# Kernel optimization log

Measured on AMD Instinct MI355X. Metric: run time of the kernel, lower is better.

The kernel has to match this reference:

```python
import jax, jax.numpy as jnp
import numpy as np

AVG_FRAMES_PER_PHONE = 8.0


def setup_inputs() -> dict:
    key = jax.random.key(0)
    k1, k2, k3 = jax.random.split(key, 3)
    B, K, D, T = 16, 512, 256, 4096
    # positive durations averaging ~8 frames per phoneme
    durations = jax.random.uniform(k1, (B, K), dtype=jnp.float32) * (2.0 * AVG_FRAMES_PER_PHONE)
    phoneme = jax.random.normal(k2, (B, D, K), dtype=jnp.float32)
    frame = jax.random.normal(k3, (B, D, T), dtype=jnp.float32)
    return {"durations": durations, "phoneme": phoneme, "frame": frame}


def reference(durations, phoneme, frame):
    """Learnable duration upsampler (NaturalSpeech-style soft alignment).

    durations: (B, K) float frames per phoneme
    phoneme:   (B, D, K)
    frame:     (B, D, T)
    """
    T = frame.shape[-1]
    acc = jnp.cumsum(durations, axis=-1)                 # (B, K) end boundaries
    centers = acc - 0.5 * durations                      # (B, K) phoneme centers
    t = jnp.arange(T, dtype=durations.dtype) + 0.5       # (T,) frame centers
    # energy: negative squared distance frame-center -> phoneme-center
    energy = -((t[None, :, None] - centers[:, None, :]) ** 2)   # (B, T, K)
    w = jax.nn.softmax(energy, axis=-1)                  # soft alignment (B, T, K)
    upsampled = jnp.einsum("btk,bdk->bdt", w, phoneme)   # (B, D, T)
    return upsampled + frame
```

## Files before the change

kernel.cpp:

```cpp
#include <hip/hip_runtime.h>
#include <hip/hip_bf16.h>

#define BK 512
#define BD 256
#define BT 4096
#define W  16
#define DSPLIT 16
#define ROWS (BD / DSPLIT)
#define SROWS 8
#define NSTAGE (ROWS / SROWS)
#define TSPAN 1024

typedef __attribute__((address_space(1))) const float gfloat;
typedef __attribute__((address_space(3))) float lfloat;
typedef float v2f __attribute__((ext_vector_type(2)));

__global__ __launch_bounds__(256, 4)
void upsampler_kernel(const float* __restrict__ durations,
                      const float* __restrict__ phoneme,
                      const float* __restrict__ frame,
                      float* __restrict__ out)
{
    const int b   = blockIdx.x;
    const int tt  = blockIdx.y;
    const int ds  = blockIdx.z;
    const int tid = threadIdx.x;

    __shared__ float s_c[BK];
    __shared__ float s_ph[2][SROWS * BK];
    __shared__ float s_wsum[4];

    const float d0v = durations[b * BK + 2 * tid];
    const float d1v = durations[b * BK + 2 * tid + 1];
    float scan = d0v + d1v;
    #pragma unroll
    for (int off = 1; off < 64; off <<= 1) {
        float other = __shfl_up(scan, off, 64);
        if ((tid & 63) >= off) scan += other;
    }
    if ((tid & 63) == 63) s_wsum[tid >> 6] = scan;
    __syncthreads();
    float woff = 0.f;
    const int wv = tid >> 6;
    for (int i = 0; i < wv; ++i) woff += s_wsum[i];
    const float acc1 = woff + scan;
    s_c[2 * tid]     = (acc1 - d1v) - 0.5f * d0v;
    s_c[2 * tid + 1] = acc1 - 0.5f * d1v;
    __syncthreads();

    const int   t0  = tt * TSPAN + 4 * tid;
    const float tcm = (float)t0 + 2.0f;

    int pos = 0;
    #pragma unroll
    for (int st = 256; st > 0; st >>= 1) {
        int np = pos + st;
        if (np <= BK && s_c[np - 1] < tcm) pos = np;
    }
    int wstart = (pos - 8) & ~3;
    wstart = max(0, min(BK - W, wstart));

    float e[4][W];
    float m[4] = {-1e30f, -1e30f, -1e30f, -1e30f};
    #pragma unroll
    for (int j = 0; j < W; ++j) {
        const float c = s_c[wstart + j];
        #pragma unroll
        for (int o = 0; o < 4; ++o) {
            float dd = ((float)t0 + 0.5f + (float)o) - c;
            e[o][j] = -dd * dd;
            m[o] = fmaxf(m[o], e[o][j]);
        }
    }
    float sum[4] = {0.f, 0.f, 0.f, 0.f};
    #pragma unroll
    for (int j = 0; j < W; ++j) {
        #pragma unroll
        for (int o = 0; o < 4; ++o) { e[o][j] = __expf(e[o][j] - m[o]); sum[o] += e[o][j]; }
    }
    v2f E[4][W / 2];
    #pragma unroll
    for (int o = 0; o < 4; ++o) {
        const float inv = 1.0f / sum[o];
        #pragma unroll
        for (int j = 0; j < W / 2; ++j)
            E[o][j] = (v2f){e[o][2 * j] * inv, e[o][2 * j + 1] * inv};
    }

    const int dlo = ds * ROWS;
    const float* phb  = phoneme + ((size_t)b * BD + dlo) * BK;
    const float* frb  = frame   + ((size_t)b * BD + dlo) * BT + (size_t)tt * TSPAN + 4 * tid;
    float*       outb = out     + ((size_t)b * BD + dlo) * BT + (size_t)tt * TSPAN + 4 * tid;

    {
        const float* gsrc = phb;
        #pragma unroll
        for (int c = 0; c < 4; ++c) {
            const int off = (c * 256 + tid) * 4;
            __builtin_amdgcn_global_load_lds((gfloat*)(gsrc + off),
                                             (lfloat*)(&s_ph[0][0] + off), 16, 0, 0);
        }
    }

    #pragma unroll
    for (int sg = 0; sg < NSTAGE; ++sg) {
        asm volatile("s_waitcnt vmcnt(0)" ::: "memory");
        __syncthreads();

        if (sg + 1 < NSTAGE) {
            const float* gsrc = phb + (size_t)(sg + 1) * SROWS * BK;
            #pragma unroll
            for (int c = 0; c < 4; ++c) {
                const int off = (c * 256 + tid) * 4;
                __builtin_amdgcn_global_load_lds((gfloat*)(gsrc + off),
                                                 (lfloat*)(&s_ph[(sg + 1) & 1][0] + off), 16, 0, 0);
            }
        }

        const float* bufp = &s_ph[sg & 1][0];
        #pragma unroll
        for (int r = 0; r < SROWS; ++r) {
            const int d = sg * SROWS + r;
            const float4 frv = *(const float4*)(frb + (size_t)d * BT);
            const float4* sp4 = (const float4*)(bufp + r * BK + wstart);
            v2f a0 = (v2f){0.f, 0.f}, a1 = a0, a2 = a0, a3 = a0;
            #pragma unroll
            for (int q = 0; q < W / 4; ++q) {
                float4 p = sp4[q];
                v2f lo = (v2f){p.x, p.y};
                v2f hi = (v2f){p.z, p.w};
                a0 = __builtin_elementwise_fma(E[0][2 * q], lo, a0);
                a0 = __builtin_elementwise_fma(E[0][2 * q + 1], hi, a0);
                a1 = __builtin_elementwise_fma(E[1][2 * q], lo, a1);
                a1 = __builtin_elementwise_fma(E[1][2 * q + 1], hi, a1);
                a2 = __builtin_elementwise_fma(E[2][2 * q], lo, a2);
                a2 = __builtin_elementwise_fma(E[2][2 * q + 1], hi, a2);
                a3 = __builtin_elementwise_fma(E[3][2 * q], lo, a3);
                a3 = __builtin_elementwise_fma(E[3][2 * q + 1], hi, a3);
            }
            float4 ov;
            ov.x = (a0.x + a0.y) + frv.x;
            ov.y = (a1.x + a1.y) + frv.y;
            ov.z = (a2.x + a2.y) + frv.z;
            ov.w = (a3.x + a3.y) + frv.w;
            *(float4*)(outb + (size_t)d * BT) = ov;
        }
    }
}

extern "C" void kernel_launch(void* const* d_in, const int* in_sizes, int n_in,
                              void* d_out, int out_size, void* d_ws, size_t ws_size,
                              hipStream_t stream) {
    const float* durations = (const float*)d_in[0];
    const float* phoneme   = (const float*)d_in[1];
    const float* frame     = (const float*)d_in[2];
    float* out = (float*)d_out;

    dim3 grid(16, BT / TSPAN, DSPLIT);
    upsampler_kernel<<<grid, 256, 0, stream>>>(durations, phoneme, frame, out);
}
```

Measured before the change: 127.1 us.

## Use 512-thread blocks with 2 frames per thread and single-stage phoneme load

Blocks grow to 512 threads, each handling 2 frame positions instead of 4, and the D dimension is split 32 ways so each block owns 8 rows. The phoneme slice is loaded into LDS in one shot, issued before the duration scan so it overlaps that work, replacing the double-buffered staged pipeline. Frame and output traffic moves from float4 to float2 accesses. The aim is more parallelism, fewer registers per thread and less synchronisation. The softmax weights are now computed by twice as many threads, and the narrower memory accesses may lower bandwidth efficiency.

```diff
diff --git a/kernel.cpp b/kernel.cpp
--- a/kernel.cpp
+++ b/kernel.cpp
@@ -1,21 +1,19 @@
 #include <hip/hip_runtime.h>
-#include <hip/hip_bf16.h>
 
 #define BK 512
 #define BD 256
 #define BT 4096
 #define W  16
-#define DSPLIT 16
+#define DSPLIT 32
 #define ROWS (BD / DSPLIT)
-#define SROWS 8
-#define NSTAGE (ROWS / SROWS)
-#define TSPAN 1024
+#define NTHR 512
+#define TSPAN (NTHR * 2)
 
 typedef __attribute__((address_space(1))) const float gfloat;
 typedef __attribute__((address_space(3))) float lfloat;
 typedef float v2f __attribute__((ext_vector_type(2)));
 
-__global__ __launch_bounds__(256, 4)
+__global__ __launch_bounds__(NTHR, 8)
 void upsampler_kernel(const float* __restrict__ durations,
                       const float* __restrict__ phoneme,
                       const float* __restrict__ frame,
@@ -27,12 +25,21 @@
     const int tid = threadIdx.x;
 
     __shared__ float s_c[BK];
-    __shared__ float s_ph[2][SROWS * BK];
-    __shared__ float s_wsum[4];
+    __shared__ float s_ph[ROWS * BK];
+    __shared__ float s_wsum[8];
 
-    const float d0v = durations[b * BK + 2 * tid];
-    const float d1v = durations[b * BK + 2 * tid + 1];
-    float scan = d0v + d1v;
+    const float d0v = durations[b * BK + tid];
+
+    const int dlo = ds * ROWS;
+    const float* phb = phoneme + ((size_t)b * BD + dlo) * BK;
+    #pragma unroll
+    for (int c = 0; c < 2; ++c) {
+        const int off = (c * NTHR + tid) * 4;
+        __builtin_amdgcn_global_load_lds((gfloat*)(phb + off),
+                                         (lfloat*)(&s_ph[0] + off), 16, 0, 0);
+    }
+
+    float scan = d0v;
     #pragma unroll
     for (int off = 1; off < 64; off <<= 1) {
         float other = __shfl_up(scan, off, 64);
@@ -43,13 +50,12 @@
     float woff = 0.f;
     const int wv = tid >> 6;
     for (int i = 0; i < wv; ++i) woff += s_wsum[i];
-    const float acc1 = woff + scan;
-    s_c[2 * tid]     = (acc1 - d1v) - 0.5f * d0v;
-    s_c[2 * tid + 1] = acc1 - 0.5f * d1v;
+    const float acc = woff + scan;
+    s_c[tid] = acc - 0.5f * d0v;
     __syncthreads();
 
-    const int   t0  = tt * TSPAN + 4 * tid;
-    const float tcm = (float)t0 + 2.0f;
+    const int   t0  = tt * TSPAN + 2 * tid;
+    const float tcm = (float)t0 + 1.0f;
 
     int pos = 0;
     #pragma unroll
@@ -60,91 +66,57 @@
     int wstart = (pos - 8) & ~3;
     wstart = max(0, min(BK - W, wstart));
 
-    float e[4][W];
-    float m[4] = {-1e30f, -1e30f, -1e30f, -1e30f};
+    float e0[W], e1[W];
+    float m0 = -1e30f, m1 = -1e30f;
     #pragma unroll
     for (int j = 0; j < W; ++j) {
         const float c = s_c[wstart + j];
-        #pragma unroll
-        for (int o = 0; o < 4; ++o) {
-            float dd = ((float)t0 + 0.5f + (float)o) - c;
-            e[o][j] = -dd * dd;
-            m[o] = fmaxf(m[o], e[o][j]);
-        }
+        const float da = ((float)t0 + 0.5f) - c;
+        const float db = da + 1.0f;
+        e0[j] = -da * da; m0 = fmaxf(m0, e0[j]);
+        e1[j] = -db * db; m1 = fmaxf(m1, e1[j]);
     }
-    float sum[4] = {0.f, 0.f, 0.f, 0.f};
+    float s0 = 0.f, s1 = 0.f;
     #pragma unroll
     for (int j = 0; j < W; ++j) {
+        e0[j] = __expf(e0[j] - m0); s0 += e0[j];
+        e1[j] = __expf(e1[j] - m1); s1 += e1[j];
+    }
+    v2f E0[W / 2], E1[W / 2];
+    {
+        const float i0 = 1.0f / s0, i1 = 1.0f / s1;
         #pragma unroll
-        for (int o = 0; o < 4; ++o) { e[o][j] = __expf(e[o][j] - m[o]); sum[o] += e[o][j]; }
-    }
-    v2f E[4][W / 2];
-    #pragma unroll
-    for (int o = 0; o < 4; ++o) {
-        const float inv = 1.0f / sum[o];
-        #pragma unroll
-        for (int j = 0; j < W / 2; ++j)
-            E[o][j] = (v2f){e[o][2 * j] * inv, e[o][2 * j + 1] * inv};
-    }
-
-    const int dlo = ds * ROWS;
-    const float* phb  = phoneme + ((size_t)b * BD + dlo) * BK;
-    const float* frb  = frame   + ((size_t)b * BD + dlo) * BT + (size_t)tt * TSPAN + 4 * tid;
-    float*       outb = out     + ((size_t)b * BD + dlo) * BT + (size_t)tt * TSPAN + 4 * tid;
-
-    {
-        const float* gsrc = phb;
-        #pragma unroll
-        for (int c = 0; c < 4; ++c) {
-            const int off = (c * 256 + tid) * 4;
-            __builtin_amdgcn_global_load_lds((gfloat*)(gsrc + off),
-                                             (lfloat*)(&s_ph[0][0] + off), 16, 0, 0);
+        for (int j = 0; j < W / 2; ++j) {
+            E0[j] = (v2f){e0[2 * j] * i0, e0[2 * j + 1] * i0};
+            E1[j] = (v2f){e1[2 * j] * i1, e1[2 * j + 1] * i1};
         }
     }
 
+    const float* frb  = frame + ((size_t)b * BD + dlo) * BT + (size_t)tt * TSPAN + 2 * tid;
+    float*       outb = out   + ((size_t)b * BD + dlo) * BT + (size_t)tt * TSPAN + 2 * tid;
+
+    asm volatile("s_waitcnt vmcnt(0)" ::: "memory");
+    __syncthreads();
+
     #pragma unroll
-    for (int sg = 0; sg < NSTAGE; ++sg) {
-        asm volatile("s_waitcnt vmcnt(0)" ::: "memory");
-        __syncthreads();
-
-        if (sg + 1 < NSTAGE) {
-            const float* gsrc = phb + (size_t)(sg + 1) * SROWS * BK;
-            #pragma unroll
-            for (int c = 0; c < 4; ++c) {
-                const int off = (c * 256 + tid) * 4;
-                __builtin_amdgcn_global_load_lds((gfloat*)(gsrc + off),
-                                                 (lfloat*)(&s_ph[(sg + 1) & 1][0] + off), 16, 0, 0);
-            }
+    for (int r = 0; r < ROWS; ++r) {
+        const float2 frv = *(const float2*)(frb + (size_t)r * BT);
+        const float4* sp4 = (const float4*)(&s_ph[r * BK + wstart]);
+        v2f a0 = (v2f){0.f, 0.f}, a1 = a0;
+        #pragma unroll
+        for (int q = 0; q < W / 4; ++q) {
+            float4 p = sp4[q];
+            v2f lo = (v2f){p.x, p.y};
+            v2f hi = (v2f){p.z, p.w};
+            a0 = __builtin_elementwise_fma(E0[2 * q],     lo, a0);
+            a0 = __builtin_elementwise_fma(E0[2 * q + 1], hi, a0);
+            a1 = __builtin_elementwise_fma(E1[2 * q],     lo, a1);
+            a1 = __builtin_elementwise_fma(E1[2 * q + 1], hi, a1);
         }
-
-        const float* bufp = &s_ph[sg & 1][0];
-        #pragma unroll
-        for (int r = 0; r < SROWS; ++r) {
-            const int d = sg * SROWS + r;
-            const float4 frv = *(const float4*)(frb + (size_t)d * BT);
-            const float4* sp4 = (const float4*)(bufp + r * BK + wstart);
-            v2f a0 = (v2f){0.f, 0.f}, a1 = a0, a2 = a0, a3 = a0;
-            #pragma unroll
-            for (int q = 0; q < W / 4; ++q) {
-                float4 p = sp4[q];
-                v2f lo = (v2f){p.x, p.y};
-                v2f hi = (v2f){p.z, p.w};
-                a0 = __builtin_elementwise_fma(E[0][2 * q], lo, a0);
-                a0 = __builtin_elementwise_fma(E[0][2 * q + 1], hi, a0);
-                a1 = __builtin_elementwise_fma(E[1][2 * q], lo, a1);
-                a1 = __builtin_elementwise_fma(E[1][2 * q + 1], hi, a1);
-                a2 = __builtin_elementwise_fma(E[2][2 * q], lo, a2);
-                a2 = __builtin_elementwise_fma(E[2][2 * q + 1], hi, a2);
-                a3 = __builtin_elementwise_fma(E[3][2 * q], lo, a3);
-                a3 = __builtin_elementwise_fma(E[3][2 * q + 1], hi, a3);
-            }
-            float4 ov;
-            ov.x = (a0.x + a0.y) + frv.x;
-            ov.y = (a1.x + a1.y) + frv.y;
-            ov.z = (a2.x + a2.y) + frv.z;
-            ov.w = (a3.x + a3.y) + frv.w;
-            *(float4*)(outb + (size_t)d * BT) = ov;
-        }
+        float2 ov;
+        ov.x = (a0.x + a0.y) + frv.x;
+        ov.y = (a1.x + a1.y) + frv.y;
+        *(float2*)(outb + (size_t)r * BT) = ov;
     }
 }
 
@@ -157,5 +129,5 @@
     float* out = (float*)d_out;
 
     dim3 grid(16, BT / TSPAN, DSPLIT);
-    upsampler_kernel<<<grid, 256, 0, stream>>>(durations, phoneme, frame, out);
+    upsampler_kernel<<<grid, NTHR, 0, stream>>>(durations, phoneme, frame, out);
 }
```

Measured after the change: 127.2 us. No clear change (+0.0%).
